# Kernel tuning notes

Hardware: AMD Instinct MI355X
Metric: run time of the kernel (lower is better)

## Reference

```python
import jax, jax.numpy as jnp
import numpy as np

B, T, C, H = 4, 2048, 1024, 16
D = C // H  # head_size = 64


def _layernorm(x, g, b, eps=1e-5):
    mu = jnp.mean(x, axis=-1, keepdims=True)
    var = jnp.var(x, axis=-1, keepdims=True)
    return (x - mu) * jax.lax.rsqrt(var + eps) * g + b


def setup_inputs() -> dict:
    key = jax.random.key(0)
    ks = jax.random.split(key, 12)
    s = 0.02
    return {
        "x": jax.random.normal(ks[0], (B, T, C), dtype=jnp.float32),
        "Wq": jax.random.normal(ks[1], (C, C), dtype=jnp.float32) * s,
        "Wk": jax.random.normal(ks[2], (C, C), dtype=jnp.float32) * s,
        "Wv": jax.random.normal(ks[3], (C, C), dtype=jnp.float32) * s,
        "Wo": jax.random.normal(ks[4], (C, C), dtype=jnp.float32) * s,
        "bo": jnp.zeros((C,), dtype=jnp.float32),
        "ln1_g": jnp.ones((C,), dtype=jnp.float32),
        "ln1_b": jnp.zeros((C,), dtype=jnp.float32),
        "ln2_g": jnp.ones((C,), dtype=jnp.float32),
        "ln2_b": jnp.zeros((C,), dtype=jnp.float32),
        "W1": jax.random.normal(ks[5], (C, 4 * C), dtype=jnp.float32) * s,
        "b1": jnp.zeros((4 * C,), dtype=jnp.float32),
        "W2": jax.random.normal(ks[6], (4 * C, C), dtype=jnp.float32) * s,
        "b2": jnp.zeros((C,), dtype=jnp.float32),
    }


def reference(x, Wq, Wk, Wv, Wo, bo, ln1_g, ln1_b, ln2_g, ln2_b, W1, b1, W2, b2):
    # --- self-attention branch (pre-LN) ---
    h = _layernorm(x, ln1_g, ln1_b)
    q = (h @ Wq).reshape(B, T, H, D)
    k = (h @ Wk).reshape(B, T, H, D)
    v = (h @ Wv).reshape(B, T, H, D)
    scores = jnp.einsum("bqhd,bkhd->bhqk", q, k) * (D ** -0.5)
    causal = jnp.tril(jnp.ones((T, T), dtype=bool))
    scores = jnp.where(causal, scores, -jnp.inf)
    attn = jax.nn.softmax(scores, axis=-1)  # dropout=0 in eval
    out = jnp.einsum("bhqk,bkhd->bqhd", attn, v).reshape(B, T, C)
    x = x + (out @ Wo + bo)
    # --- feed-forward branch (pre-LN) ---
    h2 = _layernorm(x, ln2_g, ln2_b)
    ff = jax.nn.relu(h2 @ W1 + b1) @ W2 + b2
    return x + ff
```

## Files before the change

kernel.cpp:

```cpp
#include <hip/hip_runtime.h>
#include <hip/hip_bf16.h>
#include <math.h>

#define Bsz 4
#define Tsz 2048
#define Csz 1024
#define Hsz 16
#define Dsz 64
#define Msz (Bsz * Tsz)

typedef __attribute__((ext_vector_type(8))) __bf16 bf16x8;
typedef __attribute__((ext_vector_type(2))) __bf16 bf16x2;
typedef __attribute__((ext_vector_type(4))) float f32x4;

#define GLOBAL_AS __attribute__((address_space(1)))
#define LDS_AS    __attribute__((address_space(3)))

#if __has_builtin(__builtin_amdgcn_exp2f)
#define EXP2F(x) __builtin_amdgcn_exp2f(x)
#define HAVE_NATIVE_EXP2 1
#else
#define HAVE_NATIVE_EXP2 0
#endif


__device__ __forceinline__ float block_sum256(float v, float* sh) {
#pragma unroll
    for (int o = 32; o > 0; o >>= 1) v += __shfl_down(v, o, 64);
    int lane = threadIdx.x & 63, w = threadIdx.x >> 6;
    __syncthreads();
    if (lane == 0) sh[w] = v;
    __syncthreads();
    return sh[0] + sh[1] + sh[2] + sh[3];
}


__global__ __launch_bounds__(256) void layernorm_bf16(const float* __restrict__ x,
                                                      const float* __restrict__ g,
                                                      const float* __restrict__ b,
                                                      __bf16* __restrict__ out) {
    __shared__ float sh[4];
    const int row = blockIdx.x;
    const float* xr = x + (size_t)row * Csz;
    float v[4];
    float s = 0.f, ss = 0.f;
#pragma unroll
    for (int i = 0; i < 4; i++) {
        v[i] = xr[threadIdx.x + i * 256];
        s += v[i];
        ss += v[i] * v[i];
    }
    float tot = block_sum256(s, sh);
    float mean = tot * (1.0f / Csz);
    float tot2 = block_sum256(ss, sh);
    float var = tot2 * (1.0f / Csz) - mean * mean;
    float inv = rsqrtf(var + 1e-5f);
    __bf16* orow = out + (size_t)row * Csz;
#pragma unroll
    for (int i = 0; i < 4; i++) {
        int c = threadIdx.x + i * 256;
        orow[c] = (__bf16)((v[i] - mean) * inv * g[c] + b[c]);
    }
}


__global__ __launch_bounds__(256) void transpose_bf16(const float* __restrict__ W,
                                                      __bf16* __restrict__ Wt,
                                                      int K, int N) {
    __shared__ float t[32][33];
    const int k0 = blockIdx.y * 32, n0 = blockIdx.x * 32;
    const int c = threadIdx.x & 31, r8 = threadIdx.x >> 5;
#pragma unroll
    for (int it = 0; it < 4; it++) {
        int r = r8 + it * 8;
        t[r][c] = W[(size_t)(k0 + r) * N + n0 + c];
    }
    __syncthreads();
#pragma unroll
    for (int it = 0; it < 4; it++) {
        int r = r8 + it * 8;
        Wt[(size_t)(n0 + r) * K + k0 + c] = (__bf16)t[c][r];
    }
}

__global__ __launch_bounds__(256) void transpose4_bf16(const float* __restrict__ Wa,
                                                       const float* __restrict__ Wb,
                                                       const float* __restrict__ Wc,
                                                       const float* __restrict__ Wd,
                                                       __bf16* __restrict__ Ta,
                                                       __bf16* __restrict__ Tb,
                                                       __bf16* __restrict__ Tc,
                                                       __bf16* __restrict__ Td) {
    __shared__ float t[32][33];
    const float* W = (blockIdx.z == 0) ? Wa : (blockIdx.z == 1) ? Wb : (blockIdx.z == 2) ? Wc : Wd;
    __bf16* Wt = (blockIdx.z == 0) ? Ta : (blockIdx.z == 1) ? Tb : (blockIdx.z == 2) ? Tc : Td;
    const int k0 = blockIdx.y * 32, n0 = blockIdx.x * 32;
    const int c = threadIdx.x & 31, r8 = threadIdx.x >> 5;
#pragma unroll
    for (int it = 0; it < 4; it++) {
        int r = r8 + it * 8;
        t[r][c] = W[(size_t)(k0 + r) * Csz + n0 + c];
    }
    __syncthreads();
#pragma unroll
    for (int it = 0; it < 4; it++) {
        int r = r8 + it * 8;
        Wt[(size_t)(n0 + r) * Csz + k0 + c] = (__bf16)t[c][r];
    }
}


__global__ __launch_bounds__(256) void gemm_bf16(const __bf16* __restrict__ A,
                                                 const __bf16* __restrict__ Bt,
                                                 float* __restrict__ Cf,
                                                 float* __restrict__ Cf2,
                                                 __bf16* __restrict__ Cb,
                                                 int M, int N, int K, int ld,
                                                 const float* __restrict__ bias,
                                                 const float* __restrict__ resid,
                                                 int do_relu) {
    __shared__ __bf16 As[128 * 64];
    __shared__ __bf16 Bs[128 * 64];

    const int tid = threadIdx.x;
    const int lane = tid & 63;
    const int w = tid >> 6;

    const int nwg = (int)(gridDim.x * gridDim.y);
    const int did = (int)(blockIdx.y * gridDim.x + blockIdx.x);
    const int work = ((nwg & 7) == 0) ? ((did & 7) * (nwg >> 3) + (did >> 3)) : did;
    const int bx = work % (int)gridDim.x;
    const int by = work / (int)gridDim.x;

    const int rowBase = by * 128;
    const int colBase = bx * 128;
    const int wr = (w & 1) * 64;
    const int wc = (w >> 1) * 64;

    const __bf16* Ak = A + (size_t)blockIdx.z * K;
    const __bf16* Bk = Bt + (size_t)blockIdx.z * K;
    float* Cfu = Cf;
    const float* residu = resid;
    const float* biasu = bias;
    if (blockIdx.z == 1) { Cfu = Cf2; residu = nullptr; biasu = nullptr; }

    const int m16 = lane & 15;
    const int kg = lane >> 4;
    const int swz = m16 & 7;

    const int sr = lane >> 3;
    const int sc = lane & 7;
    const int gcs = sc ^ sr;

    f32x4 acc[4][4] = {};

    for (int k0 = 0; k0 < K; k0 += 64) {
        __syncthreads();
#pragma unroll
        for (int it = 0; it < 4; it++) {
            int lr = w * 32 + it * 8;
            const __bf16* ga = Ak + (size_t)(rowBase + lr + sr) * ld + k0 + gcs * 8;
            __builtin_amdgcn_global_load_lds((const GLOBAL_AS unsigned int*)ga,
                                             (LDS_AS unsigned int*)(As + lr * 64),
                                             16, 0, 0);
            const __bf16* gb = Bk + (size_t)(colBase + lr + sr) * ld + k0 + gcs * 8;
            __builtin_amdgcn_global_load_lds((const GLOBAL_AS unsigned int*)gb,
                                             (LDS_AS unsigned int*)(Bs + lr * 64),
                                             16, 0, 0);
        }
        __syncthreads();

#pragma unroll
        for (int s = 0; s < 2; s++) {
            const int slot = ((s * 4 + kg) ^ swz) * 8;
            bf16x8 af[4], bfv[4];
#pragma unroll
            for (int i = 0; i < 4; i++)
                af[i] = *(const bf16x8*)(As + (wr + i * 16 + m16) * 64 + slot);
#pragma unroll
            for (int j = 0; j < 4; j++)
                bfv[j] = *(const bf16x8*)(Bs + (wc + j * 16 + m16) * 64 + slot);
#pragma unroll
            for (int i = 0; i < 4; i++)
#pragma unroll
                for (int j = 0; j < 4; j++)
                    acc[i][j] = __builtin_amdgcn_mfma_f32_16x16x32_bf16(af[i], bfv[j], acc[i][j], 0, 0, 0);
        }
    }

    const int cn = lane & 15;
    const int rq = (lane >> 4) * 4;
    float bj[4];
#pragma unroll
    for (int j = 0; j < 4; j++)
        bj[j] = biasu ? biasu[colBase + wc + j * 16 + cn] : 0.f;

#pragma unroll
    for (int i = 0; i < 4; i++) {
#pragma unroll
        for (int r = 0; r < 4; r++) {
            int m = rowBase + wr + i * 16 + rq + r;
            size_t rowOff = (size_t)m * N;
#pragma unroll
            for (int j = 0; j < 4; j++) {
                int n = colBase + wc + j * 16 + cn;
                float v = acc[i][j][r] + bj[j];
                if (do_relu) v = fmaxf(v, 0.f);
                if (residu) v += residu[rowOff + n];
                if (Cfu) Cfu[rowOff + n] = v;
                if (Cb && blockIdx.z == 0) Cb[rowOff + n] = (__bf16)v;
            }
        }
    }
}


#define Tile256 (256 * 64)

#define STAGE_A6(kt, hh) do {                                                      \
    const int bbuf_ = (kt) & 1;                                                    \
    _Pragma("unroll") for (int l_ = 0; l_ < 2; l_++) {                             \
        const int lr_ = (hh) * 128 + w * 16 + l_ * 8;                              \
        const __bf16* ga_ = Ak + (size_t)(rowBase + lr_ + sr) * ld + (kt) * 64 + gcs * 8; \
        __builtin_amdgcn_global_load_lds((const GLOBAL_AS unsigned int*)ga_,       \
            (LDS_AS unsigned int*)(As + bbuf_ * Tile256 + lr_ * 64), 16, 0, 0);    \
    } } while (0)

#define STAGE_B6(kt, hh) do {                                                      \
    const int bbuf_ = (kt) & 1;                                                    \
    _Pragma("unroll") for (int l_ = 0; l_ < 2; l_++) {                             \
        const int lr_ = (hh) * 128 + w * 16 + l_ * 8;                              \
        const __bf16* gb_ = Bk + (size_t)(colBase + lr_ + sr) * ld + (kt) * 64 + gcs * 8; \
        __builtin_amdgcn_global_load_lds((const GLOBAL_AS unsigned int*)gb_,       \
            (LDS_AS unsigned int*)(Bs + bbuf_ * Tile256 + lr_ * 64), 16, 0, 0);    \
    } } while (0)

#define PHASE6(ks, q, bufc, STAGES, VMW) do {                                      \
    bf16x8 af[4];                                                                  \
    _Pragma("unroll") for (int i_ = 0; i_ < 4; i_++)                               \
        af[i_] = *(const bf16x8*)(As + (bufc) * Tile256 +                          \
                  (wm * 128 + ((q) * 4 + i_) * 16 + m16) * 64 +                    \
                  ((((ks) * 4 + kg) ^ swz) * 8));                                  \
    if ((q) == 0) {                                                                \
        _Pragma("unroll") for (int j_ = 0; j_ < 4; j_++)                           \
            bv[j_] = *(const bf16x8*)(Bs + (bufc) * Tile256 +                      \
                      (wn * 64 + j_ * 16 + m16) * 64 +                             \
                      ((((ks) * 4 + kg) ^ swz) * 8));                              \
    }                                                                              \
    STAGES;                                                                        \
    VMW;                                                                           \
    __builtin_amdgcn_s_barrier();                                                  \
    __builtin_amdgcn_s_setprio(1);                                                 \
    _Pragma("unroll") for (int i_ = 0; i_ < 4; i_++)                               \
        _Pragma("unroll") for (int j_ = 0; j_ < 4; j_++)                           \
            acc[(q) * 4 + i_][j_] = __builtin_amdgcn_mfma_f32_16x16x32_bf16(       \
                af[i_], bv[j_], acc[(q) * 4 + i_][j_], 0, 0, 0);                   \
    __builtin_amdgcn_s_setprio(0);                                                 \
    __builtin_amdgcn_s_barrier();                                                  \
} while (0)

__global__ __launch_bounds__(512, 2) void gemm256(const __bf16* __restrict__ A,
                                                  const __bf16* __restrict__ Bt,
                                                  float* __restrict__ Cf,
                                                  float* __restrict__ Cf2,
                                                  __bf16* __restrict__ Cb,
                                                  int M, int N, int K, int ld,
                                                  const float* __restrict__ bias,
                                                  const float* __restrict__ resid,
                                                  int do_relu) {
    __shared__ __bf16 As[2 * Tile256];
    __shared__ __bf16 Bs[2 * Tile256];

    const int tid = threadIdx.x;
    const int lane = tid & 63;
    const int w = tid >> 6;
    const int wm = w >> 2;
    const int wn = w & 3;

    const int nwg = (int)(gridDim.x * gridDim.y);
    const int did = (int)(blockIdx.y * gridDim.x + blockIdx.x);
    const int work = ((nwg & 7) == 0) ? ((did & 7) * (nwg >> 3) + (did >> 3)) : did;
    const int bx = work % (int)gridDim.x;
    const int by = work / (int)gridDim.x;
    const int rowBase = by * 256;
    const int colBase = bx * 256;

    const __bf16* Ak = A + (size_t)blockIdx.z * K;
    const __bf16* Bk = Bt + (size_t)blockIdx.z * K;
    float* Cfu = Cf;
    const float* residu = resid;
    const float* biasu = bias;
    if (blockIdx.z == 1) { Cfu = Cf2; residu = nullptr; biasu = nullptr; }

    const int m16 = lane & 15;
    const int kg = lane >> 4;
    const int swz = m16 & 7;
    const int sr = lane >> 3;
    const int sc = lane & 7;
    const int gcs = sc ^ sr;

    const int nt = K >> 6;

    f32x4 acc[8][4] = {};
    bf16x8 bv[4];

    STAGE_A6(0, 0); STAGE_B6(0, 0); STAGE_A6(0, 1); STAGE_B6(0, 1);
    STAGE_B6(1, 0);
    asm volatile("s_waitcnt vmcnt(2)" ::: "memory");
    __builtin_amdgcn_s_barrier();

    for (int t0 = 0; t0 < nt; t0 += 2) {
        const bool p2 = (t0 + 2 < nt);
        const bool p3 = (t0 + 3 < nt);
        PHASE6(0, 0, 0, STAGE_A6(t0 + 1, 0), );
        PHASE6(0, 1, 0, STAGE_B6(t0 + 1, 1), );
        PHASE6(1, 0, 0, STAGE_A6(t0 + 1, 1), );
        PHASE6(1, 1, 0, if (p2) STAGE_B6(t0 + 2, 0),
               if (p2) asm volatile("s_waitcnt vmcnt(2)" ::: "memory");
               else    asm volatile("s_waitcnt vmcnt(0)" ::: "memory"));
        PHASE6(0, 0, 1, if (p2) STAGE_A6(t0 + 2, 0), );
        PHASE6(0, 1, 1, if (p2) STAGE_B6(t0 + 2, 1), );
        PHASE6(1, 0, 1, if (p2) STAGE_A6(t0 + 2, 1), );
        PHASE6(1, 1, 1, if (p3) STAGE_B6(t0 + 3, 0),
               if (p3) asm volatile("s_waitcnt vmcnt(2)" ::: "memory");
               else    asm volatile("s_waitcnt vmcnt(0)" ::: "memory"));
    }

    const int cn = lane & 15;
    const int rqe = (lane >> 4) * 4;
    float bj[4];
#pragma unroll
    for (int j = 0; j < 4; j++)
        bj[j] = biasu ? biasu[colBase + wn * 64 + j * 16 + cn] : 0.f;

#pragma unroll
    for (int mi = 0; mi < 8; mi++) {
#pragma unroll
        for (int r = 0; r < 4; r++) {
            const int m = rowBase + wm * 128 + mi * 16 + rqe + r;
            const size_t rowOff = (size_t)m * N;
#pragma unroll
            for (int j = 0; j < 4; j++) {
                const int n = colBase + wn * 64 + j * 16 + cn;
                float v = acc[mi][j][r] + bj[j];
                if (do_relu) v = fmaxf(v, 0.f);
                if (residu) v += residu[rowOff + n];
                if (Cfu) Cfu[rowOff + n] = v;
                if (Cb && blockIdx.z == 0) Cb[rowOff + n] = (__bf16)v;
            }
        }
    }
}


__global__ __launch_bounds__(256) void add_partial(float* __restrict__ out,
                                                   const float* __restrict__ p,
                                                   const float* __restrict__ b2) {
    size_t i = ((size_t)blockIdx.x * 256 + threadIdx.x) * 4;
    float4 o = *(float4*)(out + i);
    const float4 a = *(const float4*)(p + i);
    const float4 bb = *(const float4*)(b2 + (i & (Csz - 1)));
    o.x += a.x + bb.x;
    o.y += a.y + bb.y;
    o.z += a.z + bb.z;
    o.w += a.w + bb.w;
    *(float4*)(out + i) = o;
}


__global__ __launch_bounds__(256, 3) void attn_mfma(const __bf16* __restrict__ QKV,
                                                    __bf16* __restrict__ O) {
    __shared__ __bf16 Ks[2][64 * 64];
    __shared__ __bf16 Vt[64 * 72];
    __shared__ __bf16 Ps[128 * 72];

    const int tid = threadIdx.x;
    const int lane = tid & 63;
    const int w = tid >> 6;
    const int bh = blockIdx.x;
    const int b = bh >> 4, h = bh & 15;
    const int qt = (int)gridDim.y - 1 - (int)blockIdx.y;
    const int qbase = qt * 128;
    const int ld3C = 3 * Csz;

    const __bf16* Qg = QKV + (size_t)(b * Tsz) * ld3C + h * Dsz;
    const __bf16* Kg = Qg + Csz;
    const __bf16* Vg = Qg + 2 * Csz;

    const int m16 = lane & 15;
    const int kg = lane >> 4;
    const int rq = kg * 4;
    const int wrow = w * 32;
    const int swz = m16 & 7;

    bf16x8 aq[2][2];
#pragma unroll
    for (int i = 0; i < 2; i++)
#pragma unroll
        for (int s = 0; s < 2; s++)
            aq[i][s] = *(const bf16x8*)(Qg + (size_t)(qbase + wrow + i * 16 + m16) * ld3C + (s * 4 + kg) * 8);

    const int sr = lane >> 3;
    const int sc = lane & 7;
    const int gcs = sc ^ sr;

    const int kp = (lane & 31) * 2;
    const int dg = w * 2 + (lane >> 5);

    f32x4 Oacc[2][4];
    float l_part[2][4];
#pragma unroll
    for (int i = 0; i < 2; i++)
#pragma unroll
        for (int j = 0; j < 4; j++) Oacc[i][j] = (f32x4){0.f, 0.f, 0.f, 0.f};
#pragma unroll
    for (int i = 0; i < 2; i++)
#pragma unroll
        for (int r = 0; r < 4; r++) l_part[i][r] = 0.f;

    const float CEXP = 0.18033688f;
    const int nkt = 2 * qt + 2;

#pragma unroll
    for (int it = 0; it < 2; it++) {
        int lr = w * 16 + it * 8 + sr;
        const __bf16* src = Kg + (size_t)lr * ld3C + gcs * 8;
        __builtin_amdgcn_global_load_lds((const GLOBAL_AS unsigned int*)src,
                                         (LDS_AS unsigned int*)(&Ks[0][(w * 16 + it * 8) * 64]),
                                         16, 0, 0);
    }
    bf16x8 vc0 = *(const bf16x8*)(Vg + (size_t)kp * ld3C + dg * 8);
    bf16x8 vc1 = *(const bf16x8*)(Vg + (size_t)(kp + 1) * ld3C + dg * 8);
    bf16x8 vn0, vn1;

    for (int kt = 0; kt < nkt; kt++) {
        const int cur = kt & 1;
        const int kbase = kt * 64;

        if (kt + 1 < nkt) {
            const int nb = kbase + 64;
#pragma unroll
            for (int it = 0; it < 2; it++) {
                int lr = w * 16 + it * 8 + sr;
                const __bf16* src = Kg + (size_t)(nb + lr) * ld3C + gcs * 8;
                __builtin_amdgcn_global_load_lds((const GLOBAL_AS unsigned int*)src,
                                                 (LDS_AS unsigned int*)(&Ks[cur ^ 1][(w * 16 + it * 8) * 64]),
                                                 16, 0, 0);
            }
            vn0 = *(const bf16x8*)(Vg + (size_t)(nb + kp) * ld3C + dg * 8);
            vn1 = *(const bf16x8*)(Vg + (size_t)(nb + kp + 1) * ld3C + dg * 8);
            asm volatile("s_waitcnt vmcnt(4)" ::: "memory");
        } else {
            asm volatile("s_waitcnt vmcnt(0)" ::: "memory");
        }
        __builtin_amdgcn_s_barrier();

        f32x4 S[2][4];
#pragma unroll
        for (int i = 0; i < 2; i++)
#pragma unroll
            for (int j = 0; j < 4; j++) S[i][j] = (f32x4){0.f, 0.f, 0.f, 0.f};
#pragma unroll
        for (int s = 0; s < 2; s++) {
            bf16x8 bk[4];
#pragma unroll
            for (int j = 0; j < 4; j++)
                bk[j] = *(const bf16x8*)(&Ks[cur][(j * 16 + m16) * 64 + (((s * 4 + kg) ^ swz) * 8)]);
            __builtin_amdgcn_s_setprio(1);
#pragma unroll
            for (int i = 0; i < 2; i++)
#pragma unroll
                for (int j = 0; j < 4; j++)
                    S[i][j] = __builtin_amdgcn_mfma_f32_16x16x32_bf16(aq[i][s], bk[j], S[i][j], 0, 0, 0);
            __builtin_amdgcn_s_setprio(0);
        }

        if (kt >= 2 * qt) {
#pragma unroll
            for (int i = 0; i < 2; i++)
#pragma unroll
                for (int j = 0; j < 4; j++)
#pragma unroll
                    for (int r = 0; r < 4; r++) {
                        float arg = S[i][j][r] * CEXP;
                        if (kbase + j * 16 + m16 > qbase + wrow + i * 16 + rq + r)
                            arg = -INFINITY;
#if HAVE_NATIVE_EXP2
                        float e = EXP2F(arg);
#else
                        float e = __expf(arg * 0.6931472f);
#endif
                        S[i][j][r] = e;
                        l_part[i][r] += e;
                    }
        } else {
#pragma unroll
            for (int i = 0; i < 2; i++)
#pragma unroll
                for (int j = 0; j < 4; j++)
#pragma unroll
                    for (int r = 0; r < 4; r++) {
                        float arg = S[i][j][r] * CEXP;
#if HAVE_NATIVE_EXP2
                        float e = EXP2F(arg);
#else
                        float e = __expf(arg * 0.6931472f);
#endif
                        S[i][j][r] = e;
                        l_part[i][r] += e;
                    }
        }

#pragma unroll
        for (int i = 0; i < 2; i++)
#pragma unroll
            for (int j = 0; j < 4; j++)
#pragma unroll
                for (int r = 0; r < 4; r++)
                    Ps[(wrow + i * 16 + rq + r) * 72 + j * 16 + m16] = (__bf16)S[i][j][r];
#pragma unroll
        for (int e = 0; e < 8; e++) {
            bf16x2 pr;
            pr[0] = vc0[e];
            pr[1] = vc1[e];
            *(bf16x2*)(Vt + (dg * 8 + e) * 72 + kp) = pr;
        }
        asm volatile("s_waitcnt lgkmcnt(0)" ::: "memory");
        __builtin_amdgcn_s_barrier();

#pragma unroll
        for (int s = 0; s < 2; s++) {
            bf16x8 ap[2], bvv[4];
#pragma unroll
            for (int i = 0; i < 2; i++)
                ap[i] = *(const bf16x8*)(Ps + (wrow + i * 16 + m16) * 72 + s * 32 + kg * 8);
#pragma unroll
            for (int j = 0; j < 4; j++)
                bvv[j] = *(const bf16x8*)(Vt + (j * 16 + m16) * 72 + s * 32 + kg * 8);
            __builtin_amdgcn_s_setprio(1);
#pragma unroll
            for (int i = 0; i < 2; i++)
#pragma unroll
                for (int j = 0; j < 4; j++)
                    Oacc[i][j] = __builtin_amdgcn_mfma_f32_16x16x32_bf16(ap[i], bvv[j], Oacc[i][j], 0, 0, 0);
            __builtin_amdgcn_s_setprio(0);
        }

        if (kt + 1 < nkt) { vc0 = vn0; vc1 = vn1; }
    }

#pragma unroll
    for (int i = 0; i < 2; i++) {
#pragma unroll
        for (int r = 0; r < 4; r++) {
            float l = l_part[i][r];
#pragma unroll
            for (int msk = 1; msk < 16; msk <<= 1) l += __shfl_xor(l, msk, 64);
            const float inv = 1.0f / l;
            const int qrow = qbase + wrow + i * 16 + rq + r;
            __bf16* orow = O + (size_t)(b * Tsz + qrow) * Csz + h * Dsz;
#pragma unroll
            for (int j = 0; j < 4; j++)
                orow[j * 16 + m16] = (__bf16)(Oacc[i][j][r] * inv);
        }
    }
}


extern "C" void kernel_launch(void* const* d_in, const int* in_sizes, int n_in,
                              void* d_out, int out_size, void* d_ws, size_t ws_size,
                              hipStream_t stream) {
    const float* x     = (const float*)d_in[0];
    const float* Wq    = (const float*)d_in[1];
    const float* Wk    = (const float*)d_in[2];
    const float* Wv    = (const float*)d_in[3];
    const float* Wo    = (const float*)d_in[4];
    const float* bo    = (const float*)d_in[5];
    const float* ln1_g = (const float*)d_in[6];
    const float* ln1_b = (const float*)d_in[7];
    const float* ln2_g = (const float*)d_in[8];
    const float* ln2_b = (const float*)d_in[9];
    const float* W1    = (const float*)d_in[10];
    const float* b1    = (const float*)d_in[11];
    const float* W2    = (const float*)d_in[12];
    const float* b2    = (const float*)d_in[13];
    float* out = (float*)d_out;

    const size_t MB = 1u << 20;
    char* w = (char*)d_ws;
    __bf16* h    = (__bf16*)(w + 0);
    __bf16* Wqkv = (__bf16*)(w + 16 * MB);
    __bf16* Wot  = (__bf16*)(w + 22 * MB);
    __bf16* W1t  = (__bf16*)(w + 24 * MB);
    __bf16* W2t  = (__bf16*)(w + 32 * MB);
    __bf16* QKVb = (__bf16*)(w + 40 * MB);
    __bf16* AO   = (__bf16*)(w + 88 * MB);
    __bf16* ff1  = (__bf16*)(w + 40 * MB);
    float*  p1   = (float*)(w + 0);

    transpose4_bf16<<<dim3(32, 32, 4), 256, 0, stream>>>(Wq, Wk, Wv, Wo,
                                                         Wqkv, Wqkv + 1024 * 1024, Wqkv + 2048 * 1024, Wot);
    transpose_bf16<<<dim3(4 * Csz / 32, Csz / 32), 256, 0, stream>>>(W1, W1t, Csz, 4 * Csz);
    transpose_bf16<<<dim3(Csz / 32, 4 * Csz / 32), 256, 0, stream>>>(W2, W2t, 4 * Csz, Csz);

    layernorm_bf16<<<Msz, 256, 0, stream>>>(x, ln1_g, ln1_b, h);
    gemm256<<<dim3(3 * Csz / 256, Msz / 256), 512, 0, stream>>>(
        h, Wqkv, nullptr, nullptr, QKVb, Msz, 3 * Csz, Csz, Csz, nullptr, nullptr, 0);
    attn_mfma<<<dim3(Bsz * Hsz, Tsz / 128), 256, 0, stream>>>(QKVb, AO);
    gemm_bf16<<<dim3(Csz / 128, Msz / 128), 256, 0, stream>>>(
        AO, Wot, out, nullptr, nullptr, Msz, Csz, Csz, Csz, bo, x, 0);

    layernorm_bf16<<<Msz, 256, 0, stream>>>(out, ln2_g, ln2_b, h);
    gemm256<<<dim3(4 * Csz / 256, Msz / 256), 512, 0, stream>>>(
        h, W1t, nullptr, nullptr, ff1, Msz, 4 * Csz, Csz, Csz, b1, nullptr, 1);
    gemm256<<<dim3(Csz / 256, Msz / 256, 2), 512, 0, stream>>>(
        ff1, W2t, out, p1, nullptr, Msz, Csz, 2 * Csz, 4 * Csz, nullptr, out, 0);
    add_partial<<<Msz * Csz / 1024, 256, 0, stream>>>(out, p1, b2);
}
```

Measured before the change: 524.4 us.

## Load K fragments directly to registers and double-buffer V transpose tile

```diff
diff --git a/kernel.cpp b/kernel.cpp
--- a/kernel.cpp
+++ b/kernel.cpp
@@ -370,8 +370,7 @@
 
 __global__ __launch_bounds__(256, 3) void attn_mfma(const __bf16* __restrict__ QKV,
                                                     __bf16* __restrict__ O) {
-    __shared__ __bf16 Ks[2][64 * 64];
-    __shared__ __bf16 Vt[64 * 72];
+    __shared__ __bf16 Vt[2][64 * 72];
     __shared__ __bf16 Ps[128 * 72];
 
     const int tid = threadIdx.x;
@@ -391,7 +390,6 @@
     const int kg = lane >> 4;
     const int rq = kg * 4;
     const int wrow = w * 32;
-    const int swz = m16 & 7;
 
     bf16x8 aq[2][2];
 #pragma unroll
@@ -400,10 +398,6 @@
         for (int s = 0; s < 2; s++)
             aq[i][s] = *(const bf16x8*)(Qg + (size_t)(qbase + wrow + i * 16 + m16) * ld3C + (s * 4 + kg) * 8);
 
-    const int sr = lane >> 3;
-    const int sc = lane & 7;
-    const int gcs = sc ^ sr;
-
     const int kp = (lane & 31) * 2;
     const int dg = w * 2 + (lane >> 5);
 
@@ -421,39 +415,30 @@
     const float CEXP = 0.18033688f;
     const int nkt = 2 * qt + 2;
 
-#pragma unroll
-    for (int it = 0; it < 2; it++) {
-        int lr = w * 16 + it * 8 + sr;
-        const __bf16* src = Kg + (size_t)lr * ld3C + gcs * 8;
-        __builtin_amdgcn_global_load_lds((const GLOBAL_AS unsigned int*)src,
-                                         (LDS_AS unsigned int*)(&Ks[0][(w * 16 + it * 8) * 64]),
-                                         16, 0, 0);
-    }
+    bf16x8 bkc[2][4], bkn[2][4];
+#pragma unroll
+    for (int s = 0; s < 2; s++)
+#pragma unroll
+        for (int j = 0; j < 4; j++)
+            bkc[s][j] = *(const bf16x8*)(Kg + (size_t)(j * 16 + m16) * ld3C + (s * 4 + kg) * 8);
     bf16x8 vc0 = *(const bf16x8*)(Vg + (size_t)kp * ld3C + dg * 8);
     bf16x8 vc1 = *(const bf16x8*)(Vg + (size_t)(kp + 1) * ld3C + dg * 8);
     bf16x8 vn0, vn1;
 
     for (int kt = 0; kt < nkt; kt++) {
-        const int cur = kt & 1;
+        const int vb = kt & 1;
         const int kbase = kt * 64;
 
         if (kt + 1 < nkt) {
             const int nb = kbase + 64;
 #pragma unroll
-            for (int it = 0; it < 2; it++) {
-                int lr = w * 16 + it * 8 + sr;
-                const __bf16* src = Kg + (size_t)(nb + lr) * ld3C + gcs * 8;
-                __builtin_amdgcn_global_load_lds((const GLOBAL_AS unsigned int*)src,
-                                                 (LDS_AS unsigned int*)(&Ks[cur ^ 1][(w * 16 + it * 8) * 64]),
-                                                 16, 0, 0);
-            }
+            for (int s = 0; s < 2; s++)
+#pragma unroll
+                for (int j = 0; j < 4; j++)
+                    bkn[s][j] = *(const bf16x8*)(Kg + (size_t)(nb + j * 16 + m16) * ld3C + (s * 4 + kg) * 8);
             vn0 = *(const bf16x8*)(Vg + (size_t)(nb + kp) * ld3C + dg * 8);
             vn1 = *(const bf16x8*)(Vg + (size_t)(nb + kp + 1) * ld3C + dg * 8);
-            asm volatile("s_waitcnt vmcnt(4)" ::: "memory");
-        } else {
-            asm volatile("s_waitcnt vmcnt(0)" ::: "memory");
-        }
-        __builtin_amdgcn_s_barrier();
+        }
 
         f32x4 S[2][4];
 #pragma unroll
@@ -462,16 +447,12 @@
             for (int j = 0; j < 4; j++) S[i][j] = (f32x4){0.f, 0.f, 0.f, 0.f};
 #pragma unroll
         for (int s = 0; s < 2; s++) {
-            bf16x8 bk[4];
-#pragma unroll
-            for (int j = 0; j < 4; j++)
-                bk[j] = *(const bf16x8*)(&Ks[cur][(j * 16 + m16) * 64 + (((s * 4 + kg) ^ swz) * 8)]);
             __builtin_amdgcn_s_setprio(1);
 #pragma unroll
             for (int i = 0; i < 2; i++)
 #pragma unroll
                 for (int j = 0; j < 4; j++)
-                    S[i][j] = __builtin_amdgcn_mfma_f32_16x16x32_bf16(aq[i][s], bk[j], S[i][j], 0, 0, 0);
+                    S[i][j] = __builtin_amdgcn_mfma_f32_16x16x32_bf16(aq[i][s], bkc[s][j], S[i][j], 0, 0, 0);
             __builtin_amdgcn_s_setprio(0);
         }
 
@@ -523,7 +504,7 @@
             bf16x2 pr;
             pr[0] = vc0[e];
             pr[1] = vc1[e];
-            *(bf16x2*)(Vt + (dg * 8 + e) * 72 + kp) = pr;
+            *(bf16x2*)(&Vt[vb][(dg * 8 + e) * 72 + kp]) = pr;
         }
         asm volatile("s_waitcnt lgkmcnt(0)" ::: "memory");
         __builtin_amdgcn_s_barrier();
@@ -536,7 +517,7 @@
                 ap[i] = *(const bf16x8*)(Ps + (wrow + i * 16 + m16) * 72 + s * 32 + kg * 8);
 #pragma unroll
             for (int j = 0; j < 4; j++)
-                bvv[j] = *(const bf16x8*)(Vt + (j * 16 + m16) * 72 + s * 32 + kg * 8);
+                bvv[j] = *(const bf16x8*)(&Vt[vb][(j * 16 + m16) * 72 + s * 32 + kg * 8]);
             __builtin_amdgcn_s_setprio(1);
 #pragma unroll
             for (int i = 0; i < 2; i++)
@@ -546,7 +527,15 @@
             __builtin_amdgcn_s_setprio(0);
         }
 
-        if (kt + 1 < nkt) { vc0 = vn0; vc1 = vn1; }
+        if (kt + 1 < nkt) {
+#pragma unroll
+            for (int s = 0; s < 2; s++)
+#pragma unroll
+                for (int j = 0; j < 4; j++)
+                    bkc[s][j] = bkn[s][j];
+            vc0 = vn0;
+            vc1 = vn1;
+        }
     }
 
 #pragma unroll
```

Result: slower. 816.4 us (+55.7%).

## Double-buffer LDS fragment reads to overlap with MFMA in gemm256

Applied to the files above, without the earlier changes.

```diff
diff --git a/kernel.cpp b/kernel.cpp
--- a/kernel.cpp
+++ b/kernel.cpp
@@ -235,26 +235,27 @@
             (LDS_AS unsigned int*)(Bs + bbuf_ * Tile256 + lr_ * 64), 16, 0, 0);    \
     } } while (0)
 
-#define PHASE6(ks, q, bufc, STAGES, VMW) do {                                      \
-    bf16x8 af[4];                                                                  \
-    _Pragma("unroll") for (int i_ = 0; i_ < 4; i_++)                               \
-        af[i_] = *(const bf16x8*)(As + (bufc) * Tile256 +                          \
-                  (wm * 128 + ((q) * 4 + i_) * 16 + m16) * 64 +                    \
-                  ((((ks) * 4 + kg) ^ swz) * 8));                                  \
-    if ((q) == 0) {                                                                \
-        _Pragma("unroll") for (int j_ = 0; j_ < 4; j_++)                           \
-            bv[j_] = *(const bf16x8*)(Bs + (bufc) * Tile256 +                      \
-                      (wn * 64 + j_ * 16 + m16) * 64 +                             \
-                      ((((ks) * 4 + kg) ^ swz) * 8));                              \
-    }                                                                              \
+#define PH7(bufc, ksc, qc, FA, bufn, ksn, qn, FN, DORD, STAGES, VMW) do {          \
     STAGES;                                                                        \
     VMW;                                                                           \
     __builtin_amdgcn_s_barrier();                                                  \
+    if (DORD) {                                                                    \
+        _Pragma("unroll") for (int i_ = 0; i_ < 4; i_++)                           \
+            af[FN][i_] = *(const bf16x8*)(As + (bufn) * Tile256 +                  \
+                  (wm * 128 + ((qn) * 4 + i_) * 16 + m16) * 64 +                   \
+                  ((((ksn) * 4 + kg) ^ swz) * 8));                                 \
+        if ((qn) == 0) {                                                           \
+            _Pragma("unroll") for (int j_ = 0; j_ < 4; j_++)                       \
+                bv[ksn][j_] = *(const bf16x8*)(Bs + (bufn) * Tile256 +             \
+                      (wn * 64 + j_ * 16 + m16) * 64 +                             \
+                      ((((ksn) * 4 + kg) ^ swz) * 8));                             \
+        }                                                                          \
+    }                                                                              \
     __builtin_amdgcn_s_setprio(1);                                                 \
     _Pragma("unroll") for (int i_ = 0; i_ < 4; i_++)                               \
         _Pragma("unroll") for (int j_ = 0; j_ < 4; j_++)                           \
-            acc[(q) * 4 + i_][j_] = __builtin_amdgcn_mfma_f32_16x16x32_bf16(       \
-                af[i_], bv[j_], acc[(q) * 4 + i_][j_], 0, 0, 0);                   \
+            acc[(qc) * 4 + i_][j_] = __builtin_amdgcn_mfma_f32_16x16x32_bf16(      \
+                af[FA][i_], bv[ksc][j_], acc[(qc) * 4 + i_][j_], 0, 0, 0);         \
     __builtin_amdgcn_s_setprio(0);                                                 \
     __builtin_amdgcn_s_barrier();                                                  \
 } while (0)
@@ -302,28 +303,35 @@
     const int nt = K >> 6;
 
     f32x4 acc[8][4] = {};
-    bf16x8 bv[4];
+    bf16x8 af[2][4];
+    bf16x8 bv[2][4];
 
     STAGE_A6(0, 0); STAGE_B6(0, 0); STAGE_A6(0, 1); STAGE_B6(0, 1);
     STAGE_B6(1, 0);
     asm volatile("s_waitcnt vmcnt(2)" ::: "memory");
     __builtin_amdgcn_s_barrier();
+#pragma unroll
+    for (int i = 0; i < 4; i++)
+        af[0][i] = *(const bf16x8*)(As + (wm * 128 + i * 16 + m16) * 64 + ((kg ^ swz) * 8));
+#pragma unroll
+    for (int j = 0; j < 4; j++)
+        bv[0][j] = *(const bf16x8*)(Bs + (wn * 64 + j * 16 + m16) * 64 + ((kg ^ swz) * 8));
 
     for (int t0 = 0; t0 < nt; t0 += 2) {
         const bool p2 = (t0 + 2 < nt);
         const bool p3 = (t0 + 3 < nt);
-        PHASE6(0, 0, 0, STAGE_A6(t0 + 1, 0), );
-        PHASE6(0, 1, 0, STAGE_B6(t0 + 1, 1), );
-        PHASE6(1, 0, 0, STAGE_A6(t0 + 1, 1), );
-        PHASE6(1, 1, 0, if (p2) STAGE_B6(t0 + 2, 0),
-               if (p2) asm volatile("s_waitcnt vmcnt(2)" ::: "memory");
-               else    asm volatile("s_waitcnt vmcnt(0)" ::: "memory"));
-        PHASE6(0, 0, 1, if (p2) STAGE_A6(t0 + 2, 0), );
-        PHASE6(0, 1, 1, if (p2) STAGE_B6(t0 + 2, 1), );
-        PHASE6(1, 0, 1, if (p2) STAGE_A6(t0 + 2, 1), );
-        PHASE6(1, 1, 1, if (p3) STAGE_B6(t0 + 3, 0),
-               if (p3) asm volatile("s_waitcnt vmcnt(2)" ::: "memory");
-               else    asm volatile("s_waitcnt vmcnt(0)" ::: "memory"));
+        PH7(0, 0, 0, 0,  0, 0, 1, 1, true, STAGE_A6(t0 + 1, 0), );
+        PH7(0, 0, 1, 1,  0, 1, 0, 0, true, STAGE_B6(t0 + 1, 1), );
+        PH7(0, 1, 0, 0,  0, 1, 1, 1, true, STAGE_A6(t0 + 1, 1), );
+        PH7(0, 1, 1, 1,  1, 0, 0, 0, true, if (p2) STAGE_B6(t0 + 2, 0),
+            if (p2) asm volatile("s_waitcnt vmcnt(2)" ::: "memory");
+            else    asm volatile("s_waitcnt vmcnt(0)" ::: "memory"));
+        PH7(1, 0, 0, 0,  1, 0, 1, 1, true, if (p2) STAGE_A6(t0 + 2, 0), );
+        PH7(1, 0, 1, 1,  1, 1, 0, 0, true, if (p2) STAGE_B6(t0 + 2, 1), );
+        PH7(1, 1, 0, 0,  1, 1, 1, 1, true, if (p2) STAGE_A6(t0 + 2, 1), );
+        PH7(1, 1, 1, 1,  0, 0, 0, 0, p2,   if (p3) STAGE_B6(t0 + 3, 0),
+            if (p3) asm volatile("s_waitcnt vmcnt(2)" ::: "memory");
+            else    asm volatile("s_waitcnt vmcnt(0)" ::: "memory"));
     }
 
     const int cn = lane & 15;
```

Result: slower. 860.6 us (+64.1%).
